# Kernel tuning notes

Hardware: AMD Instinct MI355X
Metric: run time of the kernel (lower is better)

The kernel has to match this reference:

```python
import jax, jax.numpy as jnp
import numpy as np

N_NODES = 100000
N_EDGES = 1600000
DIM = 64


def setup_inputs() -> dict:
    key = jax.random.key(0)
    ks = jax.random.split(key, 10)
    return {
        "h_real": jax.random.normal(ks[0], (N_NODES, DIM), dtype=jnp.float32),
        "h_imag": jax.random.normal(ks[1], (N_NODES, DIM), dtype=jnp.float32),
        "d": jax.random.uniform(ks[2], (N_NODES,), dtype=jnp.float32),
        "w_real": jax.random.normal(ks[3], (N_EDGES,), dtype=jnp.float32),
        "w_imag": jax.random.normal(ks[4], (N_EDGES,), dtype=jnp.float32),
        "src": jax.random.randint(ks[5], (N_EDGES,), 0, N_NODES, dtype=jnp.int32),
        "dst": jax.random.randint(ks[6], (N_EDGES,), 0, N_NODES, dtype=jnp.int32),
        "W1": jax.random.normal(ks[7], (DIM, DIM), dtype=jnp.float32) * (1.414 / np.sqrt(DIM)),
        "b1": jnp.zeros((DIM,), dtype=jnp.float32),
        "W2": jax.random.normal(ks[8], (DIM, DIM), dtype=jnp.float32) * (1.414 / np.sqrt(DIM)),
        "b2": jnp.zeros((DIM,), dtype=jnp.float32),
    }


def reference(h_real, h_imag, d, w_real, w_imag, src, dst, W1, b1, W2, b2):
    n = h_real.shape[0]
    # per-edge complex coefficient e = d_dst * d_src * (w_real + i w_imag)
    dd = d[dst] * d[src]                      # [E]
    e_r = (dd * w_real)[:, None]              # [E,1]
    e_i = (dd * w_imag)[:, None]              # [E,1]
    hr = h_real[src]                          # [E,D]
    hi = h_imag[src]                          # [E,D]
    # complex multiply e * h, fused single pass over edges
    m_r = e_r * hr - e_i * hi                 # [E,D]
    m_i = e_i * hr + e_r * hi                 # [E,D]
    z_real = jax.ops.segment_sum(m_r, dst, num_segments=n)  # [N,D]
    z_imag = jax.ops.segment_sum(m_i, dst, num_segments=n)  # [N,D]
    # note: original overwrites z_real first, then z_imag uses the NEW z_real
    zr = (z_real @ W1.T + b1) - (z_imag @ W2.T + b2)
    zi = (zr @ W2.T + b2) + (z_imag @ W1.T + b1)
    return zr, zi
```

## Files before the change

kernel.cpp:

```cpp
#include <hip/hip_runtime.h>
#include <hip/hip_bf16.h>

#define N_NODES 100000
#define N_EDGES 1600000
#define DIM 64

#define TILE 4096
#define B1 ((N_EDGES + TILE - 1) / TILE)
#define K1 ((N_NODES + 255) / 256)
#define NCOUNTS (K1 * B1)
#define SCAN_BLOCK 1024
#define NSB ((NCOUNTS + SCAN_BLOCK - 1) / SCAN_BLOCK)
#define PACKB4 ((N_NODES * DIM / 4 + 255) / 256)
#define PLACE_CAP 4736
#define PULLB (N_NODES / 16)

typedef __attribute__((ext_vector_type(8))) short bf16x8;
typedef __attribute__((ext_vector_type(4))) float f32x4;

#if defined(__has_builtin)
#if __has_builtin(__builtin_amdgcn_fdot2_f32_bf16)
#define HAVE_DOT2 1
typedef __attribute__((ext_vector_type(2))) __bf16 bf16x2v;
#endif
#endif


__device__ __forceinline__ unsigned pack_bf16x2(float lo, float hi) {
  unsigned ulo = (unsigned)__hip_bfloat16_raw(__float2bfloat16(lo)).x;
  unsigned uhi = (unsigned)__hip_bfloat16_raw(__float2bfloat16(hi)).x;
  return ulo | (uhi << 16);
}
__device__ __forceinline__ float unpack_lo(unsigned u) {
  return __int_as_float((int)(u << 16));
}
__device__ __forceinline__ float unpack_hi(unsigned u) {
  return __int_as_float((int)(u & 0xFFFF0000u));
}
__device__ __forceinline__ unsigned short f2bf(float x) {
  return __hip_bfloat16_raw(__float2bfloat16(x)).x;
}

__global__ __launch_bounds__(256) void setup_fused_kernel(
    const float* __restrict__ h_real, const float* __restrict__ h_imag,
    unsigned* __restrict__ hpack, const float* __restrict__ W1,
    const float* __restrict__ b1, const float* __restrict__ W2,
    const float* __restrict__ b2, unsigned short* __restrict__ At,
    float* __restrict__ cvec, const int* __restrict__ dst,
    int* __restrict__ counts) {
  const int bid = blockIdx.x;
  const int tid = threadIdx.x;
  if (bid < PACKB4) {
    const int i = bid * 256 + tid;
    const float4 hr = ((const float4*)h_real)[i];
    const float4 hi = ((const float4*)h_imag)[i];
    uint4 o;
    o.x = pack_bf16x2(hr.x, hi.x);
    o.y = pack_bf16x2(hr.y, hi.y);
    o.z = pack_bf16x2(hr.z, hi.z);
    o.w = pack_bf16x2(hr.w, hi.w);
    ((uint4*)hpack)[i] = o;
    return;
  }
  if (bid < PACKB4 + 64) {
    const int idx = (bid - PACKB4) * 256 + tid;
    if (idx < 128 * 128) {
      const int n = idx >> 7, k = idx & 127;
      float v;
      if (n < 64) {
        v = (k < 64) ? W1[n * 64 + k] : -W2[n * 64 + (k - 64)];
      } else {
        const int nn = n - 64;
        if (k < 64) {
          float s = 0.0f;
          for (int j = 0; j < 64; ++j) s += W1[j * 64 + k] * W2[nn * 64 + j];
          v = s;
        } else {
          const int kk = k - 64;
          float s = 0.0f;
          for (int j = 0; j < 64; ++j) s += W2[j * 64 + kk] * W2[nn * 64 + j];
          v = W1[nn * 64 + kk] - s;
        }
      }
      At[n * 128 + k] = f2bf(v);
    }
    if (idx < 128) {
      if (idx < 64) {
        cvec[idx] = b1[idx] - b2[idx];
      } else {
        const int nn = idx - 64;
        float s = 0.0f;
        for (int j = 0; j < 64; ++j) s += (b1[j] - b2[j]) * W2[nn * 64 + j];
        cvec[idx] = s + b1[nn] + b2[nn];
      }
    }
    return;
  }
  __shared__ int lh[K1];
  const int hb = bid - PACKB4 - 64;
  for (int i = tid; i < K1; i += 256) lh[i] = 0;
  __syncthreads();
  const int e0 = hb * TILE;
  const int e1 = min(e0 + TILE, N_EDGES);
  for (int e = e0 + tid; e < e1; e += 256) atomicAdd(&lh[dst[e] >> 8], 1);
  __syncthreads();
  for (int b = tid; b < K1; b += 256) counts[b * B1 + hb] = lh[b];
}

__global__ __launch_bounds__(SCAN_BLOCK) void scan1_kernel(
    int* __restrict__ cnt, int* __restrict__ bsum) {
  __shared__ int wsum[16];
  const int tid = threadIdx.x;
  const int lane = tid & 63;
  const int w = tid >> 6;
  const int i = blockIdx.x * SCAN_BLOCK + tid;
  const int orig = (i < NCOUNTS) ? cnt[i] : 0;
  int v = orig;
#pragma unroll
  for (int off = 1; off < 64; off <<= 1) {
    int t = __shfl_up(v, off);
    if (lane >= off) v += t;
  }
  if (lane == 63) wsum[w] = v;
  __syncthreads();
  if (w == 0) {
    int s = (lane < 16) ? wsum[lane] : 0;
#pragma unroll
    for (int off = 1; off < 16; off <<= 1) {
      int t = __shfl_up(s, off);
      if (lane >= off) s += t;
    }
    if (lane < 16) wsum[lane] = s;
  }
  __syncthreads();
  const int wex = (w == 0) ? 0 : wsum[w - 1];
  if (i < NCOUNTS) cnt[i] = wex + v - orig;
  if (tid == SCAN_BLOCK - 1) bsum[blockIdx.x] = wex + v;
}

__global__ __launch_bounds__(256) void scan2_kernel(
    const int* __restrict__ bsum, int* __restrict__ bpre) {
  __shared__ int wsum[4];
  const int tid = threadIdx.x;
  const int lane = tid & 63;
  const int w = tid >> 6;
  const int orig = (tid < NSB) ? bsum[tid] : 0;
  int v = orig;
#pragma unroll
  for (int off = 1; off < 64; off <<= 1) {
    int t = __shfl_up(v, off);
    if (lane >= off) v += t;
  }
  if (lane == 63) wsum[w] = v;
  __syncthreads();
  if (w == 0) {
    int s = (lane < 4) ? wsum[lane] : 0;
#pragma unroll
    for (int off = 1; off < 4; off <<= 1) {
      int t = __shfl_up(s, off);
      if (lane >= off) s += t;
    }
    if (lane < 4) wsum[lane] = s;
  }
  __syncthreads();
  const int wex = (w == 0) ? 0 : wsum[w - 1];
  if (tid < NSB) bpre[tid] = wex + v - orig;
}

__global__ __launch_bounds__(512) void partition_kernel(
    const int* __restrict__ src, const int* __restrict__ dst,
    const float* __restrict__ dvec,
    const float* __restrict__ w_real, const float* __restrict__ w_imag,
    const int* __restrict__ coffs, const int* __restrict__ bpre,
    unsigned long long* __restrict__ records) {
  __shared__ unsigned long long stage[TILE];
  __shared__ unsigned short sb[TILE];
  __shared__ int lhist[512];
  __shared__ int lbase[K1];
  __shared__ int lcur[K1];
  __shared__ int gbase[K1];
  __shared__ int wsum[8];
  const int tid = threadIdx.x;
  const int lane = tid & 63;
  const int w = tid >> 6;
  const int blk = blockIdx.x;
  const int e0 = blk * TILE;
  const int cnt_t = min(TILE, N_EDGES - e0);

  lhist[tid] = 0;
  __syncthreads();
  for (int j = tid; j < cnt_t; j += 512) atomicAdd(&lhist[dst[e0 + j] >> 8], 1);
  __syncthreads();
  const int myc = lhist[tid];
  int v = myc;
#pragma unroll
  for (int off = 1; off < 64; off <<= 1) {
    int t = __shfl_up(v, off);
    if (lane >= off) v += t;
  }
  if (lane == 63) wsum[w] = v;
  __syncthreads();
  if (w == 0) {
    int s = (lane < 8) ? wsum[lane] : 0;
#pragma unroll
    for (int off = 1; off < 8; off <<= 1) {
      int t = __shfl_up(s, off);
      if (lane >= off) s += t;
    }
    if (lane < 8) wsum[lane] = s;
  }
  __syncthreads();
  const int ex = v + ((w == 0) ? 0 : wsum[w - 1]) - myc;
  if (tid < K1) {
    lbase[tid] = ex;
    lcur[tid] = ex;
    const int ci = tid * B1 + blk;
    gbase[tid] = coffs[ci] + bpre[ci >> 10];
  }
  __syncthreads();

  for (int j = tid; j < cnt_t; j += 512) {
    const int e = e0 + j;
    const int t = dst[e];
    const int s = src[e];
    const int b = t >> 8;
    const float ds = dvec[s];
    const unsigned lo = (unsigned)s | ((unsigned)(t & 255) << 17);
    const unsigned hi = pack_bf16x2(ds * w_real[e], ds * w_imag[e]);
    const int r = atomicAdd(&lcur[b], 1);
    stage[r] = ((unsigned long long)hi << 32) | lo;
    sb[r] = (unsigned short)b;
  }
  __syncthreads();
  for (int i = tid; i < cnt_t; i += 512) {
    const int b = sb[i];
    records[gbase[b] + (i - lbase[b])] = stage[i];
  }
}

__global__ __launch_bounds__(256) void place_kernel(
    unsigned long long* __restrict__ records, const int* __restrict__ coffs,
    const int* __restrict__ bpre, int* __restrict__ inc) {
  const int b = blockIdx.x;
  const int tid = threadIdx.x;
  const int lane = tid & 63;
  const int w = tid >> 6;
  const int ci0 = b * B1;
  const int bstart = coffs[ci0] + bpre[ci0 >> 10];
  int bend;
  if (b == K1 - 1) {
    bend = N_EDGES;
  } else {
    const int ci1 = (b + 1) * B1;
    bend = coffs[ci1] + bpre[ci1 >> 10];
  }
  const int cnt = min(bend - bstart, PLACE_CAP);
  const int nbase = b << 8;
  const int nn = min(256, N_NODES - nbase);

  __shared__ unsigned long long stage[PLACE_CAP];
  __shared__ int ncnt[256];
  __shared__ int ncur[256];
  __shared__ int wsum[4];

  ncnt[tid] = 0;
  __syncthreads();
  for (int i = tid; i < cnt; i += 256) {
    const unsigned long long rec = records[bstart + i];
    stage[i] = rec;
    atomicAdd(&ncnt[((unsigned)rec >> 17) & 255], 1);
  }
  __syncthreads();
  const int myc = ncnt[tid];
  int v = myc;
#pragma unroll
  for (int off = 1; off < 64; off <<= 1) {
    int t = __shfl_up(v, off);
    if (lane >= off) v += t;
  }
  if (lane == 63) wsum[w] = v;
  __syncthreads();
  if (w == 0) {
    int s = (lane < 4) ? wsum[lane] : 0;
#pragma unroll
    for (int off = 1; off < 4; off <<= 1) {
      int t = __shfl_up(s, off);
      if (lane >= off) s += t;
    }
    if (lane < 4) wsum[lane] = s;
  }
  __syncthreads();
  const int incl = v + ((w == 0) ? 0 : wsum[w - 1]);
  const int base = bstart + incl - myc;
  ncur[tid] = base;
  if (tid < nn) inc[nbase + tid] = base + myc;
  __syncthreads();
  for (int i = tid; i < cnt; i += 256) {
    const unsigned long long rec = stage[i];
    const int pos = atomicAdd(&ncur[((unsigned)rec >> 17) & 255], 1);
    records[pos] = rec;
  }
}

__global__ __launch_bounds__(512, 8) void pull_fused_kernel(
    const uint2* __restrict__ records, const int* __restrict__ inc,
    const float* __restrict__ dvec, const unsigned* __restrict__ hpack,
    const unsigned short* __restrict__ At, const float* __restrict__ cvec,
    float* __restrict__ zr_out, float* __restrict__ zi_out) {
  __shared__ __align__(16) unsigned short zs[16][136];
  __shared__ __align__(16) float outbuf[16][132];
  const int tid = threadIdx.x;
  const int lane = tid & 63;
  const int wave = tid >> 6;
  const int q4 = lane >> 4;
  const int m16 = lane & 15;
  const int node0 = blockIdx.x * 16;
  const unsigned* __restrict__ hb = hpack + 4 * m16;

#if HAVE_DOT2
#define DOT2(acc, w_, h_)                                                   \
  acc = __builtin_amdgcn_fdot2_f32_bf16(__builtin_bit_cast(bf16x2v, (w_)),  \
                                        __builtin_bit_cast(bf16x2v, (h_)),  \
                                        acc, false)
#else
#define DOT2(acc, w_, h_)                                                   \
  {                                                                         \
    const float _wl = unpack_lo(w_), _wh = unpack_hi(w_);                   \
    const float _hl = unpack_lo(h_), _hh = unpack_hi(h_);                   \
    acc += _wl * _hl + _wh * _hh;                                           \
  }
#endif

#define GATH(RR) \
  (*reinterpret_cast<const uint4*>(hb + (size_t)((RR).x & 0x1FFFF) * DIM))

#define DOTS(RR, HV)                                                        \
  {                                                                         \
    const unsigned wneg = (RR).y ^ 0x80000000u;                             \
    const unsigned wswp = ((RR).y >> 16) | ((RR).y << 16);                  \
    DOT2(sr0, wneg, (HV).x); DOT2(si0, wswp, (HV).x);                       \
    DOT2(sr1, wneg, (HV).y); DOT2(si1, wswp, (HV).y);                       \
    DOT2(sr2, wneg, (HV).z); DOT2(si2, wswp, (HV).z);                       \
    DOT2(sr3, wneg, (HV).w); DOT2(si3, wswp, (HV).w);                       \
  }

  for (int j = 0; j < 2; ++j) {
    const int n = node0 + wave * 2 + j;
    const int start = (n == 0) ? 0 : inc[n - 1];
    const int end = inc[n];
    const int deg = end - start;

    float sr0 = 0.f, sr1 = 0.f, sr2 = 0.f, sr3 = 0.f;
    float si0 = 0.f, si1 = 0.f, si2 = 0.f, si3 = 0.f;

    int p = start + q4;
    const int nfull = deg >> 2;
    int i = 0;
    for (; i + 4 <= nfull; i += 4) {
      const uint2 ra = records[p];
      const uint2 rb = records[p + 4];
      const uint2 rc = records[p + 8];
      const uint2 rd = records[p + 12];
      const uint4 ha = GATH(ra);
      const uint4 hbv = GATH(rb);
      const uint4 hc = GATH(rc);
      const uint4 hd = GATH(rd);
      DOTS(ra, ha) DOTS(rb, hbv) DOTS(rc, hc) DOTS(rd, hd)
      p += 16;
    }
    for (; i + 2 <= nfull; i += 2) {
      const uint2 ra = records[p];
      const uint2 rb = records[p + 4];
      const uint4 ha = GATH(ra);
      const uint4 hbv = GATH(rb);
      DOTS(ra, ha) DOTS(rb, hbv)
      p += 8;
    }
    if (i < nfull) {
      const uint2 ra = records[p];
      const uint4 ha = GATH(ra);
      DOTS(ra, ha)
      p += 4;
    }
    if (p < end) {
      const uint2 ra = records[p];
      const uint4 ha = GATH(ra);
      DOTS(ra, ha)
    }

#define QRED(v)                  \
    v += __shfl_xor(v, 16);      \
    v += __shfl_xor(v, 32);
    QRED(sr0) QRED(sr1) QRED(sr2) QRED(sr3)
    QRED(si0) QRED(si1) QRED(si2) QRED(si3)
#undef QRED

    const float dn = dvec[n];
    if (lane < 16) {
      const int zl = wave * 2 + j;
      uint2 rv, iv;
      rv.x = pack_bf16x2(dn * sr0, dn * sr1);
      rv.y = pack_bf16x2(dn * sr2, dn * sr3);
      iv.x = pack_bf16x2(dn * si0, dn * si1);
      iv.y = pack_bf16x2(dn * si2, dn * si3);
      *reinterpret_cast<uint2*>(&zs[zl][4 * lane]) = rv;
      *reinterpret_cast<uint2*>(&zs[zl][64 + 4 * lane]) = iv;
    }
  }
#undef DOTS
#undef GATH
#undef DOT2
  __syncthreads();

  {
    const int t = wave;
    const int m = lane & 15;
    const int q = lane >> 4;

    bf16x8 a[4];
#pragma unroll
    for (int c = 0; c < 4; ++c)
      a[c] = *reinterpret_cast<const bf16x8*>(&zs[m][c * 32 + q * 8]);

    f32x4 acc = (f32x4){0.f, 0.f, 0.f, 0.f};
    const unsigned short* brow = At + (size_t)(t * 16 + m) * 128 + q * 8;
#pragma unroll
    for (int c = 0; c < 4; ++c) {
      bf16x8 bfrag = *reinterpret_cast<const bf16x8*>(brow + c * 32);
      acc = __builtin_amdgcn_mfma_f32_16x16x32_bf16(a[c], bfrag, acc, 0, 0, 0);
    }

    const int nf = t * 16 + m;
    const float bias = cvec[nf];
#pragma unroll
    for (int r = 0; r < 4; ++r) outbuf[q * 4 + r][nf] = acc[r] + bias;
  }
  __syncthreads();

  {
    const int nl = tid >> 5;
    const int c = tid & 31;
    const float4 v = *reinterpret_cast<const float4*>(
        &outbuf[nl][(c & 15) * 4 + (c >> 4) * 64]);
    float* outp = (c < 16) ? zr_out : zi_out;
    *reinterpret_cast<float4*>(
        &outp[(size_t)(node0 + nl) * 64 + (c & 15) * 4]) = v;
  }
}

extern "C" void kernel_launch(void* const* d_in, const int* in_sizes, int n_in,
                              void* d_out, int out_size, void* d_ws, size_t ws_size,
                              hipStream_t stream) {
  const float* h_real = (const float*)d_in[0];
  const float* h_imag = (const float*)d_in[1];
  const float* dvec   = (const float*)d_in[2];
  const float* w_real = (const float*)d_in[3];
  const float* w_imag = (const float*)d_in[4];
  const int*   src    = (const int*)d_in[5];
  const int*   dst    = (const int*)d_in[6];
  const float* W1     = (const float*)d_in[7];
  const float* b1     = (const float*)d_in[8];
  const float* W2     = (const float*)d_in[9];
  const float* b2     = (const float*)d_in[10];

  char* ws = (char*)d_ws;
  unsigned short* At = (unsigned short*)ws;
  float* cvec = (float*)(ws + 128 * 128 * 2);
  unsigned long long* records = (unsigned long long*)(ws + 33792);
  unsigned* hpack = (unsigned*)(ws + 33792 + (size_t)N_EDGES * 8);
  int* counts = (int*)(ws + 33792 + (size_t)N_EDGES * 8 + (size_t)N_NODES * DIM * 4);
  int* bsum = counts + NCOUNTS;
  int* bpre = bsum + NSB;
  int* inc  = bpre + NSB;

  float* zr_out = (float*)d_out;
  float* zi_out = zr_out + (size_t)N_NODES * DIM;

  setup_fused_kernel<<<PACKB4 + 64 + B1, 256, 0, stream>>>(
      h_real, h_imag, (unsigned*)hpack, W1, b1, W2, b2, At, cvec, dst, counts);
  scan1_kernel<<<NSB, SCAN_BLOCK, 0, stream>>>(counts, bsum);
  scan2_kernel<<<1, 256, 0, stream>>>(bsum, bpre);
  partition_kernel<<<B1, 512, 0, stream>>>(src, dst, dvec, w_real, w_imag,
                                           counts, bpre, records);
  place_kernel<<<K1, 256, 0, stream>>>(records, counts, bpre, inc);
  pull_fused_kernel<<<PULLB, 512, 0, stream>>>(
      (const uint2*)records, inc, dvec, hpack, At, cvec, zr_out, zi_out);
}
```

Measured before the change: 265.1 us.

## Fuse per-node placement into pull kernel using LDS bucket sort per quarter

Removes the separate place kernel and the global inc array. Each pull block now takes one quarter (64 nodes) of a 256-node bucket, scans the bucket's records twice to count and stage its own edges in LDS, then runs the gather/dot and the MFMA transform over 64 nodes. The MFMA epilogue also writes outputs directly with scalar stores instead of going through an LDS buffer. The cost is that every bucket's records are read four times by four blocks, the number of blocks drops by a factor of four, and edges past the QCAP staging capacity are silently dropped.

```diff
diff --git a/kernel.cpp b/kernel.cpp
--- a/kernel.cpp
+++ b/kernel.cpp
@@ -12,8 +12,7 @@
 #define SCAN_BLOCK 1024
 #define NSB ((NCOUNTS + SCAN_BLOCK - 1) / SCAN_BLOCK)
 #define PACKB4 ((N_NODES * DIM / 4 + 255) / 256)
-#define PLACE_CAP 4736
-#define PULLB (N_NODES / 16)
+#define QCAP 1344
 
 typedef __attribute__((ext_vector_type(8))) short bf16x8;
 typedef __attribute__((ext_vector_type(4))) float f32x4;
@@ -238,84 +237,70 @@
   }
 }
 
-__global__ __launch_bounds__(256) void place_kernel(
-    unsigned long long* __restrict__ records, const int* __restrict__ coffs,
-    const int* __restrict__ bpre, int* __restrict__ inc) {
-  const int b = blockIdx.x;
-  const int tid = threadIdx.x;
-  const int lane = tid & 63;
-  const int w = tid >> 6;
-  const int ci0 = b * B1;
-  const int bstart = coffs[ci0] + bpre[ci0 >> 10];
-  int bend;
-  if (b == K1 - 1) {
-    bend = N_EDGES;
-  } else {
-    const int ci1 = (b + 1) * B1;
-    bend = coffs[ci1] + bpre[ci1 >> 10];
-  }
-  const int cnt = min(bend - bstart, PLACE_CAP);
-  const int nbase = b << 8;
-  const int nn = min(256, N_NODES - nbase);
-
-  __shared__ unsigned long long stage[PLACE_CAP];
-  __shared__ int ncnt[256];
-  __shared__ int ncur[256];
-  __shared__ int wsum[4];
-
-  ncnt[tid] = 0;
-  __syncthreads();
-  for (int i = tid; i < cnt; i += 256) {
-    const unsigned long long rec = records[bstart + i];
-    stage[i] = rec;
-    atomicAdd(&ncnt[((unsigned)rec >> 17) & 255], 1);
-  }
-  __syncthreads();
-  const int myc = ncnt[tid];
-  int v = myc;
-#pragma unroll
-  for (int off = 1; off < 64; off <<= 1) {
-    int t = __shfl_up(v, off);
-    if (lane >= off) v += t;
-  }
-  if (lane == 63) wsum[w] = v;
-  __syncthreads();
-  if (w == 0) {
-    int s = (lane < 4) ? wsum[lane] : 0;
-#pragma unroll
-    for (int off = 1; off < 4; off <<= 1) {
-      int t = __shfl_up(s, off);
-      if (lane >= off) s += t;
-    }
-    if (lane < 4) wsum[lane] = s;
-  }
-  __syncthreads();
-  const int incl = v + ((w == 0) ? 0 : wsum[w - 1]);
-  const int base = bstart + incl - myc;
-  ncur[tid] = base;
-  if (tid < nn) inc[nbase + tid] = base + myc;
-  __syncthreads();
-  for (int i = tid; i < cnt; i += 256) {
-    const unsigned long long rec = stage[i];
-    const int pos = atomicAdd(&ncur[((unsigned)rec >> 17) & 255], 1);
-    records[pos] = rec;
-  }
-}
-
-__global__ __launch_bounds__(512, 8) void pull_fused_kernel(
-    const uint2* __restrict__ records, const int* __restrict__ inc,
+__global__ __launch_bounds__(512, 8) void pull_sorted_kernel(
+    const unsigned long long* __restrict__ records,
+    const int* __restrict__ coffs, const int* __restrict__ bpre,
     const float* __restrict__ dvec, const unsigned* __restrict__ hpack,
     const unsigned short* __restrict__ At, const float* __restrict__ cvec,
     float* __restrict__ zr_out, float* __restrict__ zi_out) {
-  __shared__ __align__(16) unsigned short zs[16][136];
-  __shared__ __align__(16) float outbuf[16][132];
+  __shared__ unsigned long long stageB[QCAP];
+  __shared__ __align__(16) unsigned short zs[64][136];
+  __shared__ int ncnt[64];
+  __shared__ int ncur[64];
+  __shared__ int ns[64];
+  __shared__ int ne[64];
   const int tid = threadIdx.x;
   const int lane = tid & 63;
   const int wave = tid >> 6;
   const int q4 = lane >> 4;
   const int m16 = lane & 15;
-  const int node0 = blockIdx.x * 16;
+  const int b256 = blockIdx.x >> 2;
+  const int qtr = blockIdx.x & 3;
+  const int nbase = b256 * 256 + qtr * 64;
   const unsigned* __restrict__ hb = hpack + 4 * m16;
+
+  const int ci0 = b256 * B1;
+  const int bstart = coffs[ci0] + bpre[ci0 >> 10];
+  int bend;
+  if (b256 == K1 - 1) {
+    bend = N_EDGES;
+  } else {
+    const int ci1 = (b256 + 1) * B1;
+    bend = coffs[ci1] + bpre[ci1 >> 10];
+  }
+
+  if (tid < 64) ncnt[tid] = 0;
+  __syncthreads();
+
+  for (int i = bstart + tid; i < bend; i += 512) {
+    const unsigned nl = ((unsigned)records[i] >> 17) & 255u;
+    if ((int)(nl >> 6) == qtr) atomicAdd(&ncnt[nl & 63], 1);
+  }
+  __syncthreads();
+
+  if (wave == 0) {
+    const int c = ncnt[lane];
+    int v = c;
+#pragma unroll
+    for (int off = 1; off < 64; off <<= 1) {
+      int t = __shfl_up(v, off);
+      if (lane >= off) v += t;
+    }
+    ns[lane] = v - c;
+    ne[lane] = v;
+    ncur[lane] = v - c;
+  }
+  __syncthreads();
+
+  for (int i = bstart + tid; i < bend; i += 512) {
+    const unsigned long long rec = records[i];
+    const unsigned nl = ((unsigned)rec >> 17) & 255u;
+    if ((int)(nl >> 6) == qtr) {
+      const int pos = atomicAdd(&ncur[nl & 63], 1);
+      if (pos < QCAP) stageB[pos] = rec;
+    }
+  }
+  __syncthreads();
 
 #if HAVE_DOT2
 #define DOT2(acc, w_, h_)                                                   \
@@ -332,35 +317,38 @@
 #endif
 
 #define GATH(RR) \
-  (*reinterpret_cast<const uint4*>(hb + (size_t)((RR).x & 0x1FFFF) * DIM))
+  (*reinterpret_cast<const uint4*>(hb + (size_t)((unsigned)(RR) & 0x1FFFF) * DIM))
 
 #define DOTS(RR, HV)                                                        \
   {                                                                         \
-    const unsigned wneg = (RR).y ^ 0x80000000u;                             \
-    const unsigned wswp = ((RR).y >> 16) | ((RR).y << 16);                  \
+    const unsigned cf = (unsigned)((RR) >> 32);                             \
+    const unsigned wneg = cf ^ 0x80000000u;                                 \
+    const unsigned wswp = (cf >> 16) | (cf << 16);                          \
     DOT2(sr0, wneg, (HV).x); DOT2(si0, wswp, (HV).x);                       \
     DOT2(sr1, wneg, (HV).y); DOT2(si1, wswp, (HV).y);                       \
     DOT2(sr2, wneg, (HV).z); DOT2(si2, wswp, (HV).z);                       \
     DOT2(sr3, wneg, (HV).w); DOT2(si3, wswp, (HV).w);                       \
   }
 
-  for (int j = 0; j < 2; ++j) {
-    const int n = node0 + wave * 2 + j;
-    const int start = (n == 0) ? 0 : inc[n - 1];
-    const int end = inc[n];
-    const int deg = end - start;
+  for (int j = 0; j < 8; ++j) {
+    const int l = wave * 8 + j;
+    const int n = nbase + l;
+    if (n >= N_NODES) break;
+    const int s = min(ns[l], QCAP);
+    const int e = min(ne[l], QCAP);
+    const int deg = e - s;
 
     float sr0 = 0.f, sr1 = 0.f, sr2 = 0.f, sr3 = 0.f;
     float si0 = 0.f, si1 = 0.f, si2 = 0.f, si3 = 0.f;
 
-    int p = start + q4;
+    int p = s + q4;
     const int nfull = deg >> 2;
     int i = 0;
     for (; i + 4 <= nfull; i += 4) {
-      const uint2 ra = records[p];
-      const uint2 rb = records[p + 4];
-      const uint2 rc = records[p + 8];
-      const uint2 rd = records[p + 12];
+      const unsigned long long ra = stageB[p];
+      const unsigned long long rb = stageB[p + 4];
+      const unsigned long long rc = stageB[p + 8];
+      const unsigned long long rd = stageB[p + 12];
       const uint4 ha = GATH(ra);
       const uint4 hbv = GATH(rb);
       const uint4 hc = GATH(rc);
@@ -369,21 +357,21 @@
       p += 16;
     }
     for (; i + 2 <= nfull; i += 2) {
-      const uint2 ra = records[p];
-      const uint2 rb = records[p + 4];
+      const unsigned long long ra = stageB[p];
+      const unsigned long long rb = stageB[p + 4];
       const uint4 ha = GATH(ra);
       const uint4 hbv = GATH(rb);
       DOTS(ra, ha) DOTS(rb, hbv)
       p += 8;
     }
     if (i < nfull) {
-      const uint2 ra = records[p];
+      const unsigned long long ra = stageB[p];
       const uint4 ha = GATH(ra);
       DOTS(ra, ha)
       p += 4;
     }
-    if (p < end) {
-      const uint2 ra = records[p];
+    if (p < e) {
+      const unsigned long long ra = stageB[p];
       const uint4 ha = GATH(ra);
       DOTS(ra, ha)
     }
@@ -397,14 +385,13 @@
 
     const float dn = dvec[n];
     if (lane < 16) {
-      const int zl = wave * 2 + j;
       uint2 rv, iv;
       rv.x = pack_bf16x2(dn * sr0, dn * sr1);
       rv.y = pack_bf16x2(dn * sr2, dn * sr3);
       iv.x = pack_bf16x2(dn * si0, dn * si1);
       iv.y = pack_bf16x2(dn * si2, dn * si3);
-      *reinterpret_cast<uint2*>(&zs[zl][4 * lane]) = rv;
-      *reinterpret_cast<uint2*>(&zs[zl][64 + 4 * lane]) = iv;
+      *reinterpret_cast<uint2*>(&zs[l][4 * lane]) = rv;
+      *reinterpret_cast<uint2*>(&zs[l][64 + 4 * lane]) = iv;
     }
   }
 #undef DOTS
@@ -413,38 +400,34 @@
   __syncthreads();
 
   {
-    const int t = wave;
     const int m = lane & 15;
     const int q = lane >> 4;
-
-    bf16x8 a[4];
-#pragma unroll
-    for (int c = 0; c < 4; ++c)
-      a[c] = *reinterpret_cast<const bf16x8*>(&zs[m][c * 32 + q * 8]);
-
-    f32x4 acc = (f32x4){0.f, 0.f, 0.f, 0.f};
-    const unsigned short* brow = At + (size_t)(t * 16 + m) * 128 + q * 8;
-#pragma unroll
-    for (int c = 0; c < 4; ++c) {
-      bf16x8 bfrag = *reinterpret_cast<const bf16x8*>(brow + c * 32);
-      acc = __builtin_amdgcn_mfma_f32_16x16x32_bf16(a[c], bfrag, acc, 0, 0, 0);
-    }
-
-    const int nf = t * 16 + m;
-    const float bias = cvec[nf];
-#pragma unroll
-    for (int r = 0; r < 4; ++r) outbuf[q * 4 + r][nf] = acc[r] + bias;
-  }
-  __syncthreads();
-
-  {
-    const int nl = tid >> 5;
-    const int c = tid & 31;
-    const float4 v = *reinterpret_cast<const float4*>(
-        &outbuf[nl][(c & 15) * 4 + (c >> 4) * 64]);
-    float* outp = (c < 16) ? zr_out : zi_out;
-    *reinterpret_cast<float4*>(
-        &outp[(size_t)(node0 + nl) * 64 + (c & 15) * 4]) = v;
+    const int ft = wave;
+#pragma unroll
+    for (int g = 0; g < 4; ++g) {
+      bf16x8 a[4];
+#pragma unroll
+      for (int c = 0; c < 4; ++c)
+        a[c] = *reinterpret_cast<const bf16x8*>(&zs[g * 16 + m][c * 32 + q * 8]);
+
+      f32x4 acc = (f32x4){0.f, 0.f, 0.f, 0.f};
+      const unsigned short* brow = At + (size_t)(ft * 16 + m) * 128 + q * 8;
+#pragma unroll
+      for (int c = 0; c < 4; ++c) {
+        bf16x8 bfrag = *reinterpret_cast<const bf16x8*>(brow + c * 32);
+        acc = __builtin_amdgcn_mfma_f32_16x16x32_bf16(a[c], bfrag, acc, 0, 0, 0);
+      }
+
+      const int nf = ft * 16 + m;
+      const float bias = cvec[nf];
+      float* outp = (nf < 64) ? zr_out : zi_out;
+      const int nnn = nf & 63;
+#pragma unroll
+      for (int r = 0; r < 4; ++r) {
+        const int node = nbase + g * 16 + q * 4 + r;
+        if (node < N_NODES) outp[(size_t)node * 64 + nnn] = acc[r] + bias;
+      }
+    }
   }
 }
 
@@ -471,7 +454,6 @@
   int* counts = (int*)(ws + 33792 + (size_t)N_EDGES * 8 + (size_t)N_NODES * DIM * 4);
   int* bsum = counts + NCOUNTS;
   int* bpre = bsum + NSB;
-  int* inc  = bpre + NSB;
 
   float* zr_out = (float*)d_out;
   float* zi_out = zr_out + (size_t)N_NODES * DIM;
@@ -482,7 +464,6 @@
   scan2_kernel<<<1, 256, 0, stream>>>(bsum, bpre);
   partition_kernel<<<B1, 512, 0, stream>>>(src, dst, dvec, w_real, w_imag,
                                            counts, bpre, records);
-  place_kernel<<<K1, 256, 0, stream>>>(records, counts, bpre, inc);
-  pull_fused_kernel<<<PULLB, 512, 0, stream>>>(
-      (const uint2*)records, inc, dvec, hpack, At, cvec, zr_out, zi_out);
-}
+  pull_sorted_kernel<<<K1 * 4, 512, 0, stream>>>(
+      records, counts, bpre, dvec, hpack, At, cvec, zr_out, zi_out);
+}
```

New measurement: 247.9 us (median of 2 runs). 1.07x faster.
